# Performance work log

Measured on AMD Instinct MI355X. Metric: run time of the kernel, lower is better.

Reference implementation:

```python
import jax, jax.numpy as jnp
import numpy as np

CH = 512
GROUPS = 8
EPS = 1e-5


def setup_inputs() -> dict:
    key = jax.random.key(0)
    ks = jax.random.split(key, 5)
    B, C, H, W = 16, CH, 32, 32
    x = jax.random.normal(ks[0], (B, C, H, W), dtype=jnp.float32)
    # GroupNorm affine params
    norm_w = jnp.ones((C,), dtype=jnp.float32)
    norm_b = jnp.zeros((C,), dtype=jnp.float32)
    # 1x1 conv == linear over channels; store weights as [out, in]
    qkv_w = jax.random.normal(ks[1], (3 * C, C), dtype=jnp.float32) * (C ** -0.5)
    qkv_b = jnp.zeros((3 * C,), dtype=jnp.float32)
    proj_w = jax.random.normal(ks[2], (C, C), dtype=jnp.float32) * (C ** -0.5)
    proj_b = jnp.zeros((C,), dtype=jnp.float32)
    return {"x": x, "norm_w": norm_w, "norm_b": norm_b,
            "qkv_w": qkv_w, "qkv_b": qkv_b,
            "proj_w": proj_w, "proj_b": proj_b}


def _group_norm(x, w, b):
    B, C, H, W = x.shape
    g = GROUPS
    xg = x.reshape(B, g, C // g, H * W)
    mean = xg.mean(axis=(2, 3), keepdims=True)
    var = xg.var(axis=(2, 3), keepdims=True)
    xn = (xg - mean) * jax.lax.rsqrt(var + EPS)
    xn = xn.reshape(B, C, H, W)
    return xn * w[None, :, None, None] + b[None, :, None, None]


def reference(x, norm_w, norm_b, qkv_w, qkv_b, proj_w, proj_b):
    B, C, H, W = x.shape
    h = _group_norm(x, norm_w, norm_b)  # [B,C,H,W]
    hs = h.reshape(B, C, H * W)  # spatial tokens along last axis
    # 1x1 conv QKV: [3C,C] @ [B,C,N] -> [B,3C,N]
    qkv = jnp.einsum('oc,bcn->bon', qkv_w, hs) + qkv_b[None, :, None]
    q, k, v = jnp.split(qkv, 3, axis=1)  # each [B,C,N]
    scale = C ** (-0.5)
    attn = jnp.einsum('bci,bcj->bij', q, k) * scale  # [B,N,N]
    attn = jax.nn.softmax(attn, axis=-1)
    out = jnp.einsum('bij,bcj->bci', attn, v)  # [B,C,N]
    out = jnp.einsum('oc,bcn->bon', proj_w, out) + proj_b[None, :, None]
    return x + out.reshape(B, C, H, W)
```

## Files before the change

### kernel.cpp

```cpp
#include <hip/hip_runtime.h>
#include <math.h>

#define Bn   16
#define Cn   512
#define Nn   1024
#define Gn   8
#define CPG  64
#define EPSf 1e-5f

typedef short           bf16x8 __attribute__((ext_vector_type(8)));
typedef float           f32x4  __attribute__((ext_vector_type(4)));
typedef unsigned short  u16;
typedef unsigned short  u16x4  __attribute__((ext_vector_type(4)));
typedef unsigned short  u16x8  __attribute__((ext_vector_type(8)));

#define TS 136

__device__ __forceinline__ u16 f2b(float f) {
  union { float f; unsigned u; } c; c.f = f;
  unsigned r = (c.u + 0x7FFFu + ((c.u >> 16) & 1u)) >> 16;
  return (u16)r;
}

__device__ __forceinline__ void g2l16(const void* g, void* l) {
  __builtin_amdgcn_global_load_lds(
      (const __attribute__((address_space(1))) unsigned int*)g,
      (__attribute__((address_space(3))) unsigned int*)l, 16, 0, 0);
}

__device__ __forceinline__ void barrier_asm() {
  asm volatile("s_barrier" ::: "memory");
}

__device__ __forceinline__ void gemm_core(u16* As, u16* Bs,
    const u16* __restrict__ A, size_t sA,
    const u16* __restrict__ B, size_t sB, int K, f32x4 acc[4][4]) {
  const int t = threadIdx.x;
  const int w = t >> 6, l = t & 63, quad = l >> 4, lr = l & 15;
  const int wm = (w >> 1) * 64, wn = (w & 1) * 64;

  const int ra = w * 16 + (l >> 2);
  const int p  = l & 3;
  const int q  = p ^ ((ra >> 1) & 3);
  const u16* gA0 = A + (size_t)ra * sA + q * 8;
  const u16* gA1 = A + (size_t)(ra + 64) * sA + q * 8;
  const u16* gB0 = B + (size_t)ra * sB + q * 8;
  const u16* gB1 = B + (size_t)(ra + 64) * sB + q * 8;
  u16* lA0 = As + ra * 32 + p * 8;
  u16* lA1 = As + (ra + 64) * 32 + p * 8;
  u16* lB0 = Bs + ra * 32 + p * 8;
  u16* lB1 = Bs + (ra + 64) * 32 + p * 8;

  for (int k0 = 0; k0 < K; k0 += 32) {
    __syncthreads();
    g2l16(gA0 + k0, lA0);
    g2l16(gA1 + k0, lA1);
    g2l16(gB0 + k0, lB0);
    g2l16(gB1 + k0, lB1);
    __syncthreads();
    bf16x8 af[4], bfr[4];
    #pragma unroll
    for (int fm = 0; fm < 4; fm++) {
      int r = wm + fm * 16 + lr;
      af[fm] = *(const bf16x8*)&As[r * 32 + ((quad ^ ((r >> 1) & 3)) << 3)];
    }
    #pragma unroll
    for (int fn = 0; fn < 4; fn++) {
      int r = wn + fn * 16 + lr;
      bfr[fn] = *(const bf16x8*)&Bs[r * 32 + ((quad ^ ((r >> 1) & 3)) << 3)];
    }
    #pragma unroll
    for (int fm = 0; fm < 4; fm++)
      #pragma unroll
      for (int fn = 0; fn < 4; fn++)
        acc[fm][fn] = __builtin_amdgcn_mfma_f32_16x16x32_bf16(
            af[fm], bfr[fn], acc[fm][fn], 0, 0, 0);
  }
}

#define GEMM_PRE()                                              \
  const int t = threadIdx.x;                                    \
  const int w = t >> 6, l = t & 63, quad = l >> 4, lr = l & 15; \
  const int wm = (w >> 1) * 64, wn = (w & 1) * 64;              \
  (void)w; (void)wm; (void)wn; (void)l;                         \
  f32x4 acc[4][4];                                              \
  { f32x4 z = {0.f, 0.f, 0.f, 0.f};                             \
    for (int i_ = 0; i_ < 4; i_++)                              \
      for (int j_ = 0; j_ < 4; j_++) acc[i_][j_] = z; }

#define TILE_FLUSH(T, DST, rowstride)                           \
  {                                                             \
    _Pragma("unroll")                                           \
    for (int k_ = 0; k_ < 4; k_++) {                            \
      int idx = threadIdx.x + 256 * k_;                         \
      int row = idx >> 4, ch = idx & 15;                        \
      u16x8 v_ = *(u16x8*)&T[row * TS + ch * 8];                \
      *(u16x8*)&(DST)[(size_t)row * (rowstride) + ch * 8] = v_; \
    }                                                           \
  }

#define SLOT 12288

__device__ __forceinline__ void core256(const u16* __restrict__ A, size_t sA,
    const u16* __restrict__ B, size_t sB, int K, u16* SH, f32x4 acc[8][4],
    int wm, int wn, int quad, int lr) {
  const int t = threadIdx.x, wv = t >> 6, l = t & 63;
  const int srow = l >> 2;
  const int sch  = ((l & 3) ^ ((l >> 3) & 3)) * 8;

  const u16* gA[4]; int lA[4];
  const u16* gB[2]; int lB[2];
  #pragma unroll
  for (int c = 0; c < 4; c++) {
    gA[c] = A + (size_t)(wv * 64 + c * 16 + srow) * sA + sch;
    lA[c] = wv * 2048 + c * 512 + l * 8;
  }
  #pragma unroll
  for (int c = 0; c < 2; c++) {
    gB[c] = B + (size_t)(wv * 32 + c * 16 + srow) * sB + sch;
    lB[c] = 8192 + wv * 1024 + c * 512 + l * 8;
  }

  u16 *sc = SH, *sn = SH + SLOT, *sf = SH + 2 * SLOT;
  #pragma unroll
  for (int c = 0; c < 4; c++) g2l16(gA[c], sc + lA[c]);
  #pragma unroll
  for (int c = 0; c < 2; c++) g2l16(gB[c], sc + lB[c]);

  const int rch = (quad ^ ((lr >> 1) & 3)) * 8;
  int aoff[8], boff[4];
  #pragma unroll
  for (int fm = 0; fm < 8; fm++) aoff[fm] = (wm + fm * 16 + lr) * 32 + rch;
  #pragma unroll
  for (int fn = 0; fn < 4; fn++) boff[fn] = 8192 + (wn + fn * 16 + lr) * 32 + rch;

  const int nt = K >> 5;
  for (int tt = 0; tt < nt; tt++) {
    if (tt + 1 < nt) {
      const int k0 = (tt + 1) * 32;
      #pragma unroll
      for (int c = 0; c < 4; c++) g2l16(gA[c] + k0, sn + lA[c]);
      #pragma unroll
      for (int c = 0; c < 2; c++) g2l16(gB[c] + k0, sn + lB[c]);
      asm volatile("s_waitcnt vmcnt(6)" ::: "memory");
    } else {
      asm volatile("s_waitcnt vmcnt(0)" ::: "memory");
    }
    barrier_asm();
    bf16x8 af[8], bfr[4];
    #pragma unroll
    for (int fm = 0; fm < 8; fm++) af[fm] = *(const bf16x8*)&sc[aoff[fm]];
    #pragma unroll
    for (int fn = 0; fn < 4; fn++) bfr[fn] = *(const bf16x8*)&sc[boff[fn]];
    __builtin_amdgcn_s_setprio(1);
    #pragma unroll
    for (int fm = 0; fm < 8; fm++)
      #pragma unroll
      for (int fn = 0; fn < 4; fn++)
        acc[fm][fn] = __builtin_amdgcn_mfma_f32_16x16x32_bf16(
            af[fm], bfr[fn], acc[fm][fn], 0, 0, 0);
    __builtin_amdgcn_s_setprio(0);
    u16* tmp = sc; sc = sn; sn = sf; sf = tmp;
  }
}

__global__ __launch_bounds__(256) void prep_k(const float* __restrict__ qkv_w,
    const float* __restrict__ proj_w, const float* __restrict__ qkv_b,
    const float* __restrict__ x, u16* __restrict__ wqk16,
    u16* __restrict__ wvT16, u16* __restrict__ pw16,
    float* __restrict__ bias2, float* __restrict__ stats) {
  __shared__ u16 T[64][68];
  __shared__ float redf[8];
  int bid = blockIdx.x, t = threadIdx.x;
  if (bid < 512) {
    int i = bid * 256 + t;
    float4 v = ((const float4*)qkv_w)[i];
    u16x4 o;
    o.x = f2b(v.x); o.y = f2b(v.y); o.z = f2b(v.z); o.w = f2b(v.w);
    ((u16x4*)wqk16)[i] = o;
  } else if (bid < 576) {
    int tile = bid - 512, tx = tile & 7, ty = tile >> 3;
    int row = t >> 4, col4 = t & 15;
    #pragma unroll
    for (int it = 0; it < 4; it++) {
      int cc = row + it * 16;
      float4 v = *(const float4*)&qkv_w[(size_t)(1024 + ty * 64 + cc) * 512 + tx * 64 + col4 * 4];
      u16x4 o;
      o.x = f2b(v.x); o.y = f2b(v.y); o.z = f2b(v.z); o.w = f2b(v.w);
      *(u16x4*)&T[cc][col4 * 4] = o;
    }
    __syncthreads();
    #pragma unroll
    for (int it = 0; it < 2; it++) {
      int ch = t + it * 256;
      int d = ch >> 3, c8 = (ch & 7) * 8;
      u16x8 o;
      #pragma unroll
      for (int j = 0; j < 8; j++) o[j] = T[c8 + j][d];
      *(u16x8*)&wvT16[(size_t)(tx * 64 + d) * 512 + ty * 64 + c8] = o;
    }
  } else if (bid < 578) {
    int m = (bid - 576) * 256 + t;
    float s = 0.f;
    for (int c = 0; c < 512; c++)
      s += proj_w[(size_t)m * 512 + c] * qkv_b[1024 + c];
    bias2[m] = s;
  } else if (bid < 1090) {
    int idx = bid - 578, bg = idx >> 2, part = idx & 3;
    const float4* xp = (const float4*)x + (size_t)bg * 16384 + part * 4096;
    float s = 0.f, ss = 0.f;
    for (int i = t; i < 4096; i += 256) {
      float4 v = xp[i];
      s  += v.x + v.y + v.z + v.w;
      ss += v.x * v.x + v.y * v.y + v.z * v.z + v.w * v.w;
    }
    #pragma unroll
    for (int off = 32; off > 0; off >>= 1) {
      s  += __shfl_down(s, off);
      ss += __shfl_down(ss, off);
    }
    int lane = t & 63, wid = t >> 6;
    if (lane == 0) { redf[wid] = s; redf[4 + wid] = ss; }
    __syncthreads();
    if (t == 0) {
      atomicAdd(&stats[bg],       redf[0] + redf[1] + redf[2] + redf[3]);
      atomicAdd(&stats[128 + bg], redf[4] + redf[5] + redf[6] + redf[7]);
    }
  } else {
    int i = (bid - 1090) * 256 + t;
    float4 v = ((const float4*)proj_w)[i];
    u16x4 o;
    o.x = f2b(v.x); o.y = f2b(v.y); o.z = f2b(v.z); o.w = f2b(v.w);
    ((u16x4*)pw16)[i] = o;
  }
}

__global__ __launch_bounds__(256) void gnw2_k(const float* __restrict__ x,
    const float* __restrict__ stats, const float* __restrict__ nw,
    const float* __restrict__ nb, const u16* __restrict__ pw16,
    const u16* __restrict__ wvT16, u16* __restrict__ W2, u16* __restrict__ hT) {
  __shared__ u16 AsBs[8192];
  int bid = blockIdx.x;
  if (bid < 16) {
    int m0 = (bid >> 2) * 128, d0 = (bid & 3) * 128;
    GEMM_PRE();
    gemm_core(AsBs, AsBs + 4096, pw16 + (size_t)m0 * 512, 512,
              wvT16 + (size_t)d0 * 512, 512, 512, acc);
    #pragma unroll
    for (int fm = 0; fm < 4; fm++) {
      int m = m0 + wm + fm * 16 + quad * 4;
      #pragma unroll
      for (int fn = 0; fn < 4; fn++) {
        int d = d0 + wn + fn * 16 + lr;
        f32x4 a = acc[fm][fn];
        W2[(size_t)(m    ) * 512 + d] = f2b(a[0]);
        W2[(size_t)(m + 1) * 512 + d] = f2b(a[1]);
        W2[(size_t)(m + 2) * 512 + d] = f2b(a[2]);
        W2[(size_t)(m + 3) * 512 + d] = f2b(a[3]);
      }
    }
    return;
  }
  int u = bid - 16;
  int b = u >> 7, rem = u & 127, c0 = (rem >> 4) * 64, n0 = (rem & 15) * 64;
  u16 (*T)[68] = (u16(*)[68])AsBs;
  int t = threadIdx.x;
  int row = t >> 4, col4 = t & 15;
  const float inv = 1.0f / 65536.0f;
  #pragma unroll
  for (int it = 0; it < 4; it++) {
    int cc = row + it * 16;
    int c  = c0 + cc;
    int bg = b * Gn + (c >> 6);
    float mean = stats[bg] * inv;
    float var  = stats[128 + bg] * inv - mean * mean;
    float rstd = rsqrtf(var + EPSf);
    float a  = nw[c] * rstd;
    float bb = nb[c] - mean * a;
    float4 xv = *(const float4*)&x[((size_t)(b * Cn + c)) * Nn + n0 + col4 * 4];
    u16x4 o;
    o.x = f2b(xv.x * a + bb); o.y = f2b(xv.y * a + bb);
    o.z = f2b(xv.z * a + bb); o.w = f2b(xv.w * a + bb);
    *(u16x4*)&T[cc][col4 * 4] = o;
  }
  __syncthreads();
  #pragma unroll
  for (int it = 0; it < 2; it++) {
    int ch = t + it * 256;
    int n  = ch >> 3, c8 = (ch & 7) * 8;
    u16x8 o;
    #pragma unroll
    for (int j = 0; j < 8; j++) o[j] = T[c8 + j][n];
    *(u16x8*)&hT[((size_t)(b * Nn + n0 + n)) * 512 + c0 + c8] = o;
  }
}

__global__ __launch_bounds__(256, 2) void qkvp_k(const u16* __restrict__ wqk16,
    const u16* __restrict__ W2, const u16* __restrict__ hT,
    const float* __restrict__ qkv_b, u16* __restrict__ qkT,
    u16* __restrict__ VP) {
  __shared__ __align__(16) u16 SH[3 * SLOT];
  int u = blockIdx.x;
  const int t = threadIdx.x;
  const int w = t >> 6, l = t & 63, quad = l >> 4, lr = l & 15;
  const int wm = (w >> 1) * 128, wn = (w & 1) * 64;
  f32x4 acc[8][4];
  { f32x4 z = {0.f, 0.f, 0.f, 0.f};
    #pragma unroll
    for (int i_ = 0; i_ < 8; i_++)
      #pragma unroll
      for (int j_ = 0; j_ < 4; j_++) acc[i_][j_] = z; }

  if (u < 512) {
    int b = u >> 5, rem = u & 31, m0 = (rem >> 3) * 256, n0 = (rem & 7) * 128;
    core256(wqk16 + (size_t)m0 * 512, 512,
            hT + (size_t)(b * Nn + n0) * 512, 512, 512, SH, acc, wm, wn, quad, lr);
    float4 bss[8];
    #pragma unroll
    for (int fm = 0; fm < 8; fm++)
      bss[fm] = *(const float4*)&qkv_b[m0 + wm + fm * 16 + quad * 4];
    u16* T = SH;
    const int hsel = wn >> 6;
    #pragma unroll
    for (int h = 0; h < 2; h++) {
      barrier_asm();
      if (hsel == h) {
        #pragma unroll
        for (int fm = 0; fm < 8; fm++) {
          int mc = wm + fm * 16 + quad * 4;
          #pragma unroll
          for (int fn = 0; fn < 4; fn++) {
            int nl = fn * 16 + lr;
            f32x4 a = acc[fm][fn];
            u16x4 pk;
            pk.x = f2b(a[0] + bss[fm].x); pk.y = f2b(a[1] + bss[fm].y);
            pk.z = f2b(a[2] + bss[fm].z); pk.w = f2b(a[3] + bss[fm].w);
            *(u16x4*)&T[nl * 264 + mc] = pk;
          }
        }
      }
      barrier_asm();
      #pragma unroll
      for (int kk = 0; kk < 8; kk++) {
        int idx = t + 256 * kk, row = idx >> 5, grp = idx & 31;
        u16x8 v = *(u16x8*)&T[row * 264 + grp * 8];
        *(u16x8*)&qkT[((size_t)(b * Nn + n0 + h * 64 + row)) * 1024 + m0 + grp * 8] = v;
      }
    }
  } else {
    int u2 = u - 512;
    int b = u2 >> 4, rem = u2 & 15, m0 = (rem >> 3) * 256, j0 = (rem & 7) * 128;
    core256(W2 + (size_t)m0 * 512, 512,
            hT + (size_t)(b * Nn + j0) * 512, 512, 512, SH, acc, wm, wn, quad, lr);
    u16* T = SH;
    const int hsel = wm >> 7;
    #pragma unroll
    for (int h = 0; h < 2; h++) {
      barrier_asm();
      if (hsel == h) {
        #pragma unroll
        for (int fm = 0; fm < 8; fm++) {
          int ml = fm * 16 + quad * 4;
          #pragma unroll
          for (int fn = 0; fn < 4; fn++) {
            int jl = wn + fn * 16 + lr;
            f32x4 a = acc[fm][fn];
            T[(ml    ) * TS + jl] = f2b(a[0]);
            T[(ml + 1) * TS + jl] = f2b(a[1]);
            T[(ml + 2) * TS + jl] = f2b(a[2]);
            T[(ml + 3) * TS + jl] = f2b(a[3]);
          }
        }
      }
      barrier_asm();
      #pragma unroll
      for (int kk = 0; kk < 8; kk++) {
        int idx = t + 256 * kk, row = idx >> 4, grp = idx & 15;
        u16x8 v = *(u16x8*)&T[row * TS + grp * 8];
        *(u16x8*)&VP[((size_t)(b * 512 + m0 + h * 128 + row)) * 1024 + j0 + grp * 8] = v;
      }
    }
  }
}

__global__ __launch_bounds__(256) void qkexp_k(const u16* __restrict__ qkT,
    u16* __restrict__ Pm, float* __restrict__ rpart) {
  __shared__ u16 SH[64 * TS];
  __shared__ float psum[128];
  int u = blockIdx.x;
  int b = u >> 6, rem = u & 63, i0 = (rem >> 3) * 128, j0 = (rem & 7) * 128;
  const u16* base = qkT + (size_t)b * Nn * 1024;
  GEMM_PRE();
  gemm_core(SH, SH + 4096, base + (size_t)i0 * 1024, 1024,
            base + (size_t)j0 * 1024 + 512, 1024, 512, acc);
  if (t < 128) psum[t] = 0.f;
  __syncthreads();
  const float scale = 0.04419417382415922f;
  #pragma unroll
  for (int fm = 0; fm < 4; fm++) {
    int ri = wm + fm * 16 + quad * 4;
    float rs0 = 0.f, rs1 = 0.f, rs2 = 0.f, rs3 = 0.f;
    #pragma unroll
    for (int fn = 0; fn < 4; fn++) {
      f32x4 a = acc[fn >= 0 ? fm : fm][fn];
      rs0 += __expf(a[0] * scale);
      rs1 += __expf(a[1] * scale);
      rs2 += __expf(a[2] * scale);
      rs3 += __expf(a[3] * scale);
    }
    #pragma unroll
    for (int mask = 1; mask < 16; mask <<= 1) {
      rs0 += __shfl_xor(rs0, mask);
      rs1 += __shfl_xor(rs1, mask);
      rs2 += __shfl_xor(rs2, mask);
      rs3 += __shfl_xor(rs3, mask);
    }
    if (lr == 0) {
      atomicAdd(&psum[ri],     rs0);
      atomicAdd(&psum[ri + 1], rs1);
      atomicAdd(&psum[ri + 2], rs2);
      atomicAdd(&psum[ri + 3], rs3);
    }
  }
  __syncthreads();
  if (t < 128)
    rpart[((size_t)(b * 8) + (rem & 7)) * 1024 + i0 + t] = psum[t];
  #pragma unroll
  for (int h = 0; h < 2; h++) {
    __syncthreads();
    if ((w >> 1) == h) {
      #pragma unroll
      for (int fm = 0; fm < 4; fm++) {
        int il = fm * 16 + quad * 4;
        #pragma unroll
        for (int fn = 0; fn < 4; fn++) {
          int jl = wn + fn * 16 + lr;
          f32x4 a = acc[fm][fn];
          SH[(il    ) * TS + jl] = f2b(__expf(a[0] * scale));
          SH[(il + 1) * TS + jl] = f2b(__expf(a[1] * scale));
          SH[(il + 2) * TS + jl] = f2b(__expf(a[2] * scale));
          SH[(il + 3) * TS + jl] = f2b(__expf(a[3] * scale));
        }
      }
    }
    __syncthreads();
    u16* dst = Pm + ((size_t)(b * Nn + i0 + h * 64)) * 1024 + j0;
    TILE_FLUSH(SH, dst, 1024);
  }
}

__global__ __launch_bounds__(256) void pvout_k(const u16* __restrict__ VP,
    const u16* __restrict__ Pm, const float* __restrict__ rpart,
    const float* __restrict__ bias2, const float* __restrict__ proj_b,
    const float* __restrict__ x, float* __restrict__ out) {
  __shared__ u16 AsBs[8192];
  __shared__ float rinv[128];
  int bid = blockIdx.x;
  int b = bid >> 5, rem = bid & 31, m0 = (rem >> 3) * 128, i0 = (rem & 7) * 128;
  if (threadIdx.x < 128) {
    float s = 0.f;
    #pragma unroll
    for (int jb = 0; jb < 8; jb++)
      s += rpart[((size_t)(b * 8 + jb)) * 1024 + i0 + threadIdx.x];
    rinv[threadIdx.x] = 1.0f / s;
  }
  GEMM_PRE();
  gemm_core(AsBs, AsBs + 4096, VP + ((size_t)(b * 512 + m0)) * 1024, 1024,
            Pm + ((size_t)(b * Nn + i0)) * 1024, 1024, 1024, acc);
  #pragma unroll
  for (int fm = 0; fm < 4; fm++) {
    int m = m0 + wm + fm * 16 + quad * 4;
    float c0 = bias2[m    ] + proj_b[m    ];
    float c1 = bias2[m + 1] + proj_b[m + 1];
    float c2 = bias2[m + 2] + proj_b[m + 2];
    float c3 = bias2[m + 3] + proj_b[m + 3];
    #pragma unroll
    for (int fn = 0; fn < 4; fn++) {
      int il = wn + fn * 16 + lr;
      int i  = i0 + il;
      float ri = rinv[il];
      f32x4 a = acc[fm][fn];
      size_t o0 = ((size_t)(b * Cn + m)) * Nn + i;
      out[o0                  ] = a[0] * ri + c0 + x[o0                  ];
      out[o0 + Nn             ] = a[1] * ri + c1 + x[o0 + Nn             ];
      out[o0 + 2 * Nn         ] = a[2] * ri + c2 + x[o0 + 2 * Nn         ];
      out[o0 + 3 * (size_t)Nn] = a[3] * ri + c3 + x[o0 + 3 * (size_t)Nn];
    }
  }
}

extern "C" void kernel_launch(void* const* d_in, const int* in_sizes, int n_in,
                              void* d_out, int out_size, void* d_ws, size_t ws_size,
                              hipStream_t stream) {
  const float* x      = (const float*)d_in[0];
  const float* norm_w = (const float*)d_in[1];
  const float* norm_b = (const float*)d_in[2];
  const float* qkv_w  = (const float*)d_in[3];
  const float* qkv_b  = (const float*)d_in[4];
  const float* proj_w = (const float*)d_in[5];
  const float* proj_b = (const float*)d_in[6];
  float* out = (float*)d_out;
  char* ws = (char*)d_ws;

  u16*   wqk16 = (u16*)(ws);
  u16*   wvT16 = (u16*)(ws + 1048576);
  u16*   pw16  = (u16*)(ws + 1572864);
  u16*   W2    = (u16*)(ws + 2097152);
  float* bias2 = (float*)(ws + 2621440);
  float* stats = (float*)(ws + 2623488);
  u16*   hT    = (u16*)(ws + 2624512);
  u16*   qkT   = (u16*)(ws + 19401728);
  u16*   VP    = (u16*)(ws + 52956160);
  u16*   Pm    = (u16*)(ws + 69733376);
  float* rpart = (float*)(ws + 103287808);

  hipMemsetAsync(stats, 0, 1024, stream);
  prep_k<<<1346, 256, 0, stream>>>(qkv_w, proj_w, qkv_b, x, wqk16, wvT16,
                                   pw16, bias2, stats);
  gnw2_k<<<2064, 256, 0, stream>>>(x, stats, norm_w, norm_b, pw16, wvT16,
                                   W2, hT);
  qkvp_k<<<768, 256, 0, stream>>>(wqk16, W2, hT, qkv_b, qkT, VP);
  qkexp_k<<<1024, 256, 0, stream>>>(qkT, Pm, rpart);
  pvout_k<<<512, 256, 0, stream>>>(VP, Pm, rpart, bias2, proj_b, x, out);
}
```

Before: 225.8 us.

## Switch QK-exp and PV-out kernels to 256x128 triple-buffered core256 tiles

The QK^T exponent kernel and the PV/output projection kernel now use the larger 256x128 core256 GEMM path with a triple-buffered LDS pipeline instead of the 128x128 double-buffered core. Grid sizes are halved accordingly, and the row-sum accumulation is fused into the exp/store pass. The aim is higher arithmetic intensity and better latency hiding per block. The cost is higher register and LDS use per block and fewer blocks, which may reduce occupancy or leave the CUs less evenly loaded.

```diff
diff --git a/kernel.cpp b/kernel.cpp
--- a/kernel.cpp
+++ b/kernel.cpp
@@ -88,17 +88,6 @@
     for (int i_ = 0; i_ < 4; i_++)                              \
       for (int j_ = 0; j_ < 4; j_++) acc[i_][j_] = z; }
 
-#define TILE_FLUSH(T, DST, rowstride)                           \
-  {                                                             \
-    _Pragma("unroll")                                           \
-    for (int k_ = 0; k_ < 4; k_++) {                            \
-      int idx = threadIdx.x + 256 * k_;                         \
-      int row = idx >> 4, ch = idx & 15;                        \
-      u16x8 v_ = *(u16x8*)&T[row * TS + ch * 8];                \
-      *(u16x8*)&(DST)[(size_t)row * (rowstride) + ch * 8] = v_; \
-    }                                                           \
-  }
-
 #define SLOT 12288
 
 __device__ __forceinline__ void core256(const u16* __restrict__ A, size_t sA,
@@ -163,6 +152,18 @@
     u16* tmp = sc; sc = sn; sn = sf; sf = tmp;
   }
 }
+
+#define CORE256_PRE()                                             \
+  const int t = threadIdx.x;                                      \
+  const int w = t >> 6, l = t & 63, quad = l >> 4, lr = l & 15;   \
+  const int wm = (w >> 1) * 128, wn = (w & 1) * 64;               \
+  (void)l;                                                        \
+  f32x4 acc[8][4];                                                \
+  { f32x4 z = {0.f, 0.f, 0.f, 0.f};                               \
+    _Pragma("unroll")                                             \
+    for (int i_ = 0; i_ < 8; i_++)                                \
+      _Pragma("unroll")                                           \
+      for (int j_ = 0; j_ < 4; j_++) acc[i_][j_] = z; }
 
 __global__ __launch_bounds__(256) void prep_k(const float* __restrict__ qkv_w,
     const float* __restrict__ proj_w, const float* __restrict__ qkv_b,
@@ -301,15 +302,7 @@
     u16* __restrict__ VP) {
   __shared__ __align__(16) u16 SH[3 * SLOT];
   int u = blockIdx.x;
-  const int t = threadIdx.x;
-  const int w = t >> 6, l = t & 63, quad = l >> 4, lr = l & 15;
-  const int wm = (w >> 1) * 128, wn = (w & 1) * 64;
-  f32x4 acc[8][4];
-  { f32x4 z = {0.f, 0.f, 0.f, 0.f};
-    #pragma unroll
-    for (int i_ = 0; i_ < 8; i_++)
-      #pragma unroll
-      for (int j_ = 0; j_ < 4; j_++) acc[i_][j_] = z; }
+  CORE256_PRE();
 
   if (u < 512) {
     int b = u >> 5, rem = u & 31, m0 = (rem >> 3) * 256, n0 = (rem & 7) * 128;
@@ -383,80 +376,78 @@
   }
 }
 
-__global__ __launch_bounds__(256) void qkexp_k(const u16* __restrict__ qkT,
+__global__ __launch_bounds__(256, 2) void qkexp_k(const u16* __restrict__ qkT,
     u16* __restrict__ Pm, float* __restrict__ rpart) {
-  __shared__ u16 SH[64 * TS];
-  __shared__ float psum[128];
+  __shared__ __align__(16) u16 SH[3 * SLOT];
+  __shared__ float psum[256];
   int u = blockIdx.x;
-  int b = u >> 6, rem = u & 63, i0 = (rem >> 3) * 128, j0 = (rem & 7) * 128;
+  int b = u >> 5, rem = u & 31, i0 = (rem >> 3) * 256, j0 = (rem & 7) * 128;
   const u16* base = qkT + (size_t)b * Nn * 1024;
-  GEMM_PRE();
-  gemm_core(SH, SH + 4096, base + (size_t)i0 * 1024, 1024,
-            base + (size_t)j0 * 1024 + 512, 1024, 512, acc);
-  if (t < 128) psum[t] = 0.f;
-  __syncthreads();
+  CORE256_PRE();
+  core256(base + (size_t)i0 * 1024, 1024,
+          base + (size_t)j0 * 1024 + 512, 1024, 512, SH, acc, wm, wn, quad, lr);
+  psum[t] = 0.f;
   const float scale = 0.04419417382415922f;
-  #pragma unroll
-  for (int fm = 0; fm < 4; fm++) {
-    int ri = wm + fm * 16 + quad * 4;
-    float rs0 = 0.f, rs1 = 0.f, rs2 = 0.f, rs3 = 0.f;
-    #pragma unroll
-    for (int fn = 0; fn < 4; fn++) {
-      f32x4 a = acc[fn >= 0 ? fm : fm][fn];
-      rs0 += __expf(a[0] * scale);
-      rs1 += __expf(a[1] * scale);
-      rs2 += __expf(a[2] * scale);
-      rs3 += __expf(a[3] * scale);
-    }
-    #pragma unroll
-    for (int mask = 1; mask < 16; mask <<= 1) {
-      rs0 += __shfl_xor(rs0, mask);
-      rs1 += __shfl_xor(rs1, mask);
-      rs2 += __shfl_xor(rs2, mask);
-      rs3 += __shfl_xor(rs3, mask);
-    }
-    if (lr == 0) {
-      atomicAdd(&psum[ri],     rs0);
-      atomicAdd(&psum[ri + 1], rs1);
-      atomicAdd(&psum[ri + 2], rs2);
-      atomicAdd(&psum[ri + 3], rs3);
-    }
-  }
-  __syncthreads();
-  if (t < 128)
-    rpart[((size_t)(b * 8) + (rem & 7)) * 1024 + i0 + t] = psum[t];
+  u16* T = SH;
+  const int hsel = wm >> 7;
   #pragma unroll
   for (int h = 0; h < 2; h++) {
-    __syncthreads();
-    if ((w >> 1) == h) {
-      #pragma unroll
-      for (int fm = 0; fm < 4; fm++) {
+    barrier_asm();
+    if (hsel == h) {
+      #pragma unroll
+      for (int fm = 0; fm < 8; fm++) {
         int il = fm * 16 + quad * 4;
+        float rs0 = 0.f, rs1 = 0.f, rs2 = 0.f, rs3 = 0.f;
         #pragma unroll
         for (int fn = 0; fn < 4; fn++) {
           int jl = wn + fn * 16 + lr;
           f32x4 a = acc[fm][fn];
-          SH[(il    ) * TS + jl] = f2b(__expf(a[0] * scale));
-          SH[(il + 1) * TS + jl] = f2b(__expf(a[1] * scale));
-          SH[(il + 2) * TS + jl] = f2b(__expf(a[2] * scale));
-          SH[(il + 3) * TS + jl] = f2b(__expf(a[3] * scale));
+          float e0 = __expf(a[0] * scale);
+          float e1 = __expf(a[1] * scale);
+          float e2 = __expf(a[2] * scale);
+          float e3 = __expf(a[3] * scale);
+          rs0 += e0; rs1 += e1; rs2 += e2; rs3 += e3;
+          T[(il    ) * TS + jl] = f2b(e0);
+          T[(il + 1) * TS + jl] = f2b(e1);
+          T[(il + 2) * TS + jl] = f2b(e2);
+          T[(il + 3) * TS + jl] = f2b(e3);
+        }
+        #pragma unroll
+        for (int mask = 1; mask < 16; mask <<= 1) {
+          rs0 += __shfl_xor(rs0, mask);
+          rs1 += __shfl_xor(rs1, mask);
+          rs2 += __shfl_xor(rs2, mask);
+          rs3 += __shfl_xor(rs3, mask);
+        }
+        if (lr == 0) {
+          int ri = h * 128 + il;
+          atomicAdd(&psum[ri],     rs0);
+          atomicAdd(&psum[ri + 1], rs1);
+          atomicAdd(&psum[ri + 2], rs2);
+          atomicAdd(&psum[ri + 3], rs3);
         }
       }
     }
-    __syncthreads();
-    u16* dst = Pm + ((size_t)(b * Nn + i0 + h * 64)) * 1024 + j0;
-    TILE_FLUSH(SH, dst, 1024);
-  }
-}
-
-__global__ __launch_bounds__(256) void pvout_k(const u16* __restrict__ VP,
+    barrier_asm();
+    #pragma unroll
+    for (int kk = 0; kk < 8; kk++) {
+      int idx = t + 256 * kk, row = idx >> 4, grp = idx & 15;
+      u16x8 v = *(u16x8*)&T[row * TS + grp * 8];
+      *(u16x8*)&Pm[((size_t)(b * Nn + i0 + h * 128 + row)) * 1024 + j0 + grp * 8] = v;
+    }
+  }
+  __syncthreads();
+  rpart[((size_t)(b * 8) + (rem & 7)) * 1024 + i0 + t] = psum[t];
+}
+
+__global__ __launch_bounds__(256, 2) void pvout_k(const u16* __restrict__ VP,
     const u16* __restrict__ Pm, const float* __restrict__ rpart,
     const float* __restrict__ bias2, const float* __restrict__ proj_b,
     const float* __restrict__ x, float* __restrict__ out) {
-  __shared__ u16 AsBs[8192];
+  __shared__ __align__(16) u16 SH[3 * SLOT];
   __shared__ float rinv[128];
   int bid = blockIdx.x;
-  int b = bid >> 5, rem = bid & 31, m0 = (rem >> 3) * 128, i0 = (rem & 7) * 128;
+  int b = bid >> 4, rem = bid & 15, m0 = (rem >> 3) * 256, i0 = (rem & 7) * 128;
   if (threadIdx.x < 128) {
     float s = 0.f;
     #pragma unroll
@@ -464,11 +455,12 @@
       s += rpart[((size_t)(b * 8 + jb)) * 1024 + i0 + threadIdx.x];
     rinv[threadIdx.x] = 1.0f / s;
   }
-  GEMM_PRE();
-  gemm_core(AsBs, AsBs + 4096, VP + ((size_t)(b * 512 + m0)) * 1024, 1024,
-            Pm + ((size_t)(b * Nn + i0)) * 1024, 1024, 1024, acc);
-  #pragma unroll
-  for (int fm = 0; fm < 4; fm++) {
+  CORE256_PRE();
+  core256(VP + ((size_t)(b * 512 + m0)) * 1024, 1024,
+          Pm + ((size_t)(b * Nn + i0)) * 1024, 1024, 1024, SH, acc, wm, wn, quad, lr);
+  __syncthreads();
+  #pragma unroll
+  for (int fm = 0; fm < 8; fm++) {
     int m = m0 + wm + fm * 16 + quad * 4;
     float c0 = bias2[m    ] + proj_b[m    ];
     float c1 = bias2[m + 1] + proj_b[m + 1];
@@ -520,6 +512,6 @@
   gnw2_k<<<2064, 256, 0, stream>>>(x, stats, norm_w, norm_b, pw16, wvT16,
                                    W2, hT);
   qkvp_k<<<768, 256, 0, stream>>>(wqk16, W2, hT, qkv_b, qkT, VP);
-  qkexp_k<<<1024, 256, 0, stream>>>(qkT, Pm, rpart);
-  pvout_k<<<512, 256, 0, stream>>>(VP, Pm, rpart, bias2, proj_b, x, out);
-}
+  qkexp_k<<<512, 256, 0, stream>>>(qkT, Pm, rpart);
+  pvout_k<<<256, 256, 0, stream>>>(VP, Pm, rpart, bias2, proj_b, x, out);
+}
```

New measurement: 228.1 us. Within noise of the previous version (+1.0%).
